# Kernel optimization log

Measured on AMD Instinct MI355X. Metric: run time of the kernel, lower is better.

## Reference

```python
import jax, jax.numpy as jnp
import numpy as np


def setup_inputs() -> dict:
    key = jax.random.key(0)
    ks = jax.random.split(key, 6)
    B, S, H = 1, 512, 2048
    NH, D = 16, 128
    S_CACHE = 8192
    TOPK = 16
    hidden_states = jax.random.normal(ks[0], (B, S, H), dtype=jnp.float32)
    Wqkv = jax.random.normal(ks[1], (3 * H, H), dtype=jnp.float32) * 0.02
    Wout = jax.random.normal(ks[2], (H, H), dtype=jnp.float32) * 0.02
    k_cache = jax.random.normal(ks[3], (B, NH, S_CACHE, D), dtype=jnp.float32)
    v_cache = jax.random.normal(ks[4], (B, NH, S_CACHE, D), dtype=jnp.float32)
    position_bias = jax.random.normal(ks[5], (NH, S, S), dtype=jnp.float32) * 0.1
    # causal mask: True = masked out (matches torch masked_fill semantics)
    attention_mask = ~jnp.tril(jnp.ones((S, S), dtype=bool))
    return {
        "hidden_states": hidden_states,
        "Wqkv": Wqkv,
        "Wout": Wout,
        "k_cache": k_cache,
        "v_cache": v_cache,
        "position_bias": position_bias,
        "attention_mask": attention_mask,
        "topk": TOPK,
    }


SIM_THRESHOLD = 0.25  # config.sim_threshold


def reference(hidden_states, Wqkv, Wout, k_cache, v_cache, position_bias,
              attention_mask, topk):
    B, S, H = hidden_states.shape
    NH, D = k_cache.shape[1], k_cache.shape[3]
    scale = 1.0 / jnp.sqrt(jnp.asarray(D, hidden_states.dtype))

    # QKV projection (Linear, no bias): x @ W^T, then split heads
    qkv = jnp.einsum('bsh,oh->bso', hidden_states, Wqkv)
    q, k, v = jnp.split(qkv, 3, axis=-1)
    def to_heads(x):
        return x.reshape(B, S, NH, D).transpose(0, 2, 1, 3)  # [B,NH,S,D]
    q, k, v = to_heads(q), to_heads(k), to_heads(v)

    # local attention scores + alibi-style bias
    scores_local = jnp.einsum('bhqd,bhkd->bhqk', q, k) * scale
    scores_local = scores_local + position_bias[None]  # [B,NH,S,S]

    # cosine-similarity retrieval over long-range cache
    q_n = q / jnp.linalg.norm(q, axis=-1, keepdims=True)
    k_n = k_cache / jnp.linalg.norm(k_cache, axis=-1, keepdims=True)
    sim = jnp.einsum('bhqd,bhkd->bhqk', q_n, k_n)  # [B,NH,S,S_CACHE]
    val, idx = jax.lax.top_k(sim, topk)            # [B,NH,S,topk]
    reshaped_idx = idx.reshape(B, NH, S * topk)

    # gather retrieved K/V
    sel_k = jnp.take_along_axis(k_cache, reshaped_idx[..., None], axis=2)  # [B,NH,S*topk,D]
    sel_v = jnp.take_along_axis(v_cache, reshaped_idx[..., None], axis=2)

    scores_cache = jnp.einsum('bhqd,bhkd->bhqk', q, sel_k) * scale  # [B,NH,S,S*topk]
    neg = jnp.finfo(scores_cache.dtype).min

    # similarity-threshold mask (mask_by_sim=True)
    sim_mask = ~(val > SIM_THRESHOLD)                       # [B,NH,S,topk]
    sim_mask = sim_mask.reshape(B, NH, 1, S * topk)         # broadcast over queries
    scores_cache = jnp.where(sim_mask, neg, scores_cache)

    # block-diagonal external-memory mask: query i attends only to its own topk slots
    rows = jnp.arange(S)[:, None]
    cols_block = jnp.arange(S * topk)[None, :] // topk
    ext_mask = cols_block != rows                           # [S, S*topk], True = masked

    full_mask = jnp.concatenate([ext_mask, attention_mask], axis=1)  # [S, S*topk+S]
    scores = jnp.concatenate([scores_cache, scores_local], axis=-1)
    scores = jnp.where(full_mask[None, None], neg, scores)

    attn = jax.nn.softmax(scores.astype(jnp.float32), axis=-1).astype(v.dtype)
    values = jnp.concatenate([sel_v, v], axis=2)            # [B,NH,S*topk+S,D]
    ctx = jnp.einsum('bhqk,bhkd->bhqd', attn, values)
    ctx = ctx.transpose(0, 2, 1, 3).reshape(B, S, H)
    attn_output = jnp.einsum('bsh,oh->bso', ctx, Wout)
    return attn_output
```

## Files before the change

### kernel.cpp

```cpp
#include <hip/hip_runtime.h>

typedef _Float16 half8 __attribute__((ext_vector_type(8)));
typedef _Float16 half4 __attribute__((ext_vector_type(4)));
typedef _Float16 half2t __attribute__((ext_vector_type(2)));
typedef float f32x4 __attribute__((ext_vector_type(4)));
typedef float f32x2 __attribute__((ext_vector_type(2)));

#define NHEAD 16
#define SEQ 512
#define DIM 128
#define HID 2048
#define SCACHE 8192
#define CAP 64
#define SCALE 0.08838834764831845f
#define NEG_INF (-__builtin_inff())

__global__ __launch_bounds__(256) void gemm_xwT(const float* __restrict__ A,
                                                const float* __restrict__ B,
                                                float* __restrict__ Cpart,
                                                int K, int gridN, int kslices) {
  __shared__ __align__(16) _Float16 As[128][84];
  __shared__ __align__(16) _Float16 Bs[128][84];
  int b = blockIdx.x;
  int kblk = b % kslices;
  int nm = b / kslices;
  int nblk = nm % gridN, mblk = nm / gridN;
  int N = gridN * 128;
  int kchunk = K / kslices;
  int t = threadIdx.x;
  int lane = t & 63, wid = t >> 6;
  int wm = (wid >> 1) * 64, wn = (wid & 1) * 64;
  f32x4 acc[4][4] = {};
  const float* Ab = A + (size_t)mblk * 128 * K;
  const float* Bb = B + (size_t)nblk * 128 * K;
  int rowS = t >> 4, c4 = (t & 15) * 4;

  for (int k0 = kblk * kchunk; k0 < kblk * kchunk + kchunk; k0 += 64) {
#pragma unroll
    for (int i = 0; i < 8; ++i) {
      int row = rowS + 16 * i;
      float4 av = *(const float4*)(Ab + (size_t)row * K + k0 + c4);
      float4 bv = *(const float4*)(Bb + (size_t)row * K + k0 + c4);
      half4 ah = {(_Float16)av.x, (_Float16)av.y, (_Float16)av.z, (_Float16)av.w};
      half4 bh = {(_Float16)bv.x, (_Float16)bv.y, (_Float16)bv.z, (_Float16)bv.w};
      *(half4*)&As[row][c4] = ah;
      *(half4*)&Bs[row][c4] = bh;
    }
    __syncthreads();
#pragma unroll
    for (int ks = 0; ks < 2; ++ks) {
      int ko = ks * 32 + (lane >> 4) * 8;
      int rr = lane & 15;
      half8 af[4], bf[4];
#pragma unroll
      for (int i = 0; i < 4; ++i) af[i] = *(const half8*)&As[wm + i * 16 + rr][ko];
#pragma unroll
      for (int j = 0; j < 4; ++j) bf[j] = *(const half8*)&Bs[wn + j * 16 + rr][ko];
#pragma unroll
      for (int i = 0; i < 4; ++i)
#pragma unroll
        for (int j = 0; j < 4; ++j)
          acc[i][j] = __builtin_amdgcn_mfma_f32_16x16x32_f16(af[i], bf[j], acc[i][j], 0, 0, 0);
    }
    __syncthreads();
  }
  float* Cp = Cpart + (size_t)kblk * ((size_t)gridN * 128) * 512;
  int cR = (lane >> 4) * 4, cC = lane & 15;
#pragma unroll
  for (int i = 0; i < 4; ++i)
#pragma unroll
    for (int j = 0; j < 4; ++j) {
      int row = mblk * 128 + wm + i * 16 + cR;
      int col = nblk * 128 + wn + j * 16 + cC;
#pragma unroll
      for (int r = 0; r < 4; ++r)
        Cp[(size_t)(row + r) * N + col] = acc[i][j][r];
    }
}

__global__ __launch_bounds__(256) void reduce_k(const float* __restrict__ part,
                                                float* __restrict__ dst,
                                                int kslices, int ncol, int dstride) {
  size_t e = ((size_t)blockIdx.x * 256 + threadIdx.x) * 4;
  size_t slice = (size_t)512 * ncol;
  f32x4 s = *(const f32x4*)(part + e);
  for (int p = 1; p < kslices; ++p)
    s += *(const f32x4*)(part + (size_t)p * slice + e);
  size_t row = e / ncol;
  int col = (int)(e % ncol);
  *(f32x4*)(dst + row * dstride + col) = s;
}

__global__ __launch_bounds__(256) void split_hilo(const float* __restrict__ src,
                                                  _Float16* __restrict__ hi,
                                                  _Float16* __restrict__ lo) {
  size_t e = ((size_t)blockIdx.x * 256 + threadIdx.x) * 4;
  f32x4 v = *(const f32x4*)(src + e);
  half4 h = {(_Float16)v[0], (_Float16)v[1], (_Float16)v[2], (_Float16)v[3]};
  half4 l = {(_Float16)(v[0] - (float)h[0]), (_Float16)(v[1] - (float)h[1]),
             (_Float16)(v[2] - (float)h[2]), (_Float16)(v[3] - (float)h[3])};
  *(half4*)(hi + e) = h;
  *(half4*)(lo + e) = l;
}

__global__ __launch_bounds__(256) void gemm_q_hi(const _Float16* __restrict__ Ahg,
                                                 const _Float16* __restrict__ Alg,
                                                 const _Float16* __restrict__ Bhg,
                                                 const _Float16* __restrict__ Blg,
                                                 float* __restrict__ C) {
  __shared__ __align__(16) _Float16 Ahs[32][72], Als[32][72];
  __shared__ __align__(16) _Float16 Bhs[32][72], Bls[32][72];
  int b = blockIdx.x;
  int nblk = b & 63, mblk = b >> 6;
  int t = threadIdx.x, lane = t & 63, w = t >> 6;
  int wm = (w >> 1) * 16, wn = (w & 1) * 16;
  int quad = lane >> 4, rr = lane & 15;
  f32x4 acc = {};
  const _Float16* Ab0 = Ahg + (size_t)(mblk * 32) * 2048;
  const _Float16* Ab1 = Alg + (size_t)(mblk * 32) * 2048;
  const _Float16* Bb0 = Bhg + (size_t)(nblk * 32) * 2048;
  const _Float16* Bb1 = Blg + (size_t)(nblk * 32) * 2048;
  int srow = t >> 3, sc = (t & 7) * 8;

  for (int k0 = 0; k0 < 2048; k0 += 64) {
    size_t goff = (size_t)srow * 2048 + k0 + sc;
    *(uint4*)&Ahs[srow][sc] = *(const uint4*)(Ab0 + goff);
    *(uint4*)&Als[srow][sc] = *(const uint4*)(Ab1 + goff);
    *(uint4*)&Bhs[srow][sc] = *(const uint4*)(Bb0 + goff);
    *(uint4*)&Bls[srow][sc] = *(const uint4*)(Bb1 + goff);
    __syncthreads();
#pragma unroll
    for (int ks = 0; ks < 2; ++ks) {
      int ko = ks * 32 + quad * 8;
      half8 afh = *(const half8*)&Ahs[wm + rr][ko];
      half8 afl = *(const half8*)&Als[wm + rr][ko];
      half8 bfh = *(const half8*)&Bhs[wn + rr][ko];
      half8 bfl = *(const half8*)&Bls[wn + rr][ko];
      acc = __builtin_amdgcn_mfma_f32_16x16x32_f16(afl, bfh, acc, 0, 0, 0);
      acc = __builtin_amdgcn_mfma_f32_16x16x32_f16(afh, bfl, acc, 0, 0, 0);
      acc = __builtin_amdgcn_mfma_f32_16x16x32_f16(afh, bfh, acc, 0, 0, 0);
    }
    __syncthreads();
  }
  int row = mblk * 32 + wm + quad * 4;
  int col = nblk * 32 + wn + rr;
#pragma unroll
  for (int r = 0; r < 4; ++r)
    C[(size_t)(row + r) * (3 * HID) + col] = acc[r];
}

__global__ __launch_bounds__(256) void cache_norm(const float* __restrict__ kc,
                                                  _Float16* __restrict__ kn16,
                                                  double* __restrict__ kninv) {
  int w = threadIdx.x >> 6, lane = threadIdx.x & 63;
  int row = blockIdx.x * 4 + w;
  f32x2 v = *(const f32x2*)(kc + (size_t)row * DIM + lane * 2);
  double s = (double)v[0] * v[0] + (double)v[1] * v[1];
#pragma unroll
  for (int off = 32; off; off >>= 1) s += __shfl_xor(s, off);
  float inv = rsqrtf((float)s);
  half2t o = {(_Float16)(v[0] * inv), (_Float16)(v[1] * inv)};
  *(half2t*)(kn16 + (size_t)row * DIM + lane * 2) = o;
  if (lane == 0) kninv[row] = 1.0 / sqrt(s);
}

__global__ __launch_bounds__(256) void prep_local(const float* __restrict__ qkv,
                                                  _Float16* __restrict__ q16,
                                                  _Float16* __restrict__ k16,
                                                  _Float16* __restrict__ qn16) {
  int w = threadIdx.x >> 6, lane = threadIdx.x & 63;
  int rid = blockIdx.x * 4 + w;
  int h = rid >> 9, s = rid & 511;
  const float* qp = qkv + (size_t)s * (3 * HID) + h * DIM + lane * 2;
  f32x2 q = *(const f32x2*)qp;
  f32x2 k = *(const f32x2*)(qp + HID);
  float ss = q[0] * q[0] + q[1] * q[1];
#pragma unroll
  for (int off = 32; off; off >>= 1) ss += __shfl_xor(ss, off);
  float inv = rsqrtf(ss);
  half2t qh = {(_Float16)q[0], (_Float16)q[1]};
  half2t kh = {(_Float16)k[0], (_Float16)k[1]};
  half2t qnh = {(_Float16)(q[0] * inv), (_Float16)(q[1] * inv)};
  *(half2t*)(q16 + (size_t)rid * DIM + lane * 2) = qh;
  *(half2t*)(k16 + (size_t)rid * DIM + lane * 2) = kh;
  *(half2t*)(qn16 + (size_t)rid * DIM + lane * 2) = qnh;
}

__global__ __launch_bounds__(256) void sim_cand(const _Float16* __restrict__ qn16,
                                                const _Float16* __restrict__ kn16,
                                                int* __restrict__ cnt,
                                                int* __restrict__ cidx) {
  __shared__ __align__(16) _Float16 Qs[64][132];
  int b = blockIdx.x;
  int h = b & 15, cblk = b >> 4;
  int t = threadIdx.x, lane = t & 63, w = t >> 6;
  int quad = lane >> 4, rr = lane & 15;

  half8 bf[2][4];
  {
    const _Float16* kb = kn16 + ((size_t)(h * SCACHE + cblk * 128 + w * 32)) * DIM;
#pragma unroll
    for (int jn = 0; jn < 2; ++jn)
#pragma unroll
      for (int ks = 0; ks < 4; ++ks)
        bf[jn][ks] = *(const half8*)(kb + (size_t)(jn * 16 + rr) * DIM + ks * 32 + quad * 8);
  }

  for (int qt = 0; qt < 8; ++qt) {
    __syncthreads();
    const _Float16* qb = qn16 + ((size_t)(h * SEQ + qt * 64)) * DIM;
#pragma unroll
    for (int i = 0; i < 4; ++i) {
      int f = t + 256 * i;
      int row = f >> 4, c8 = (f & 15) * 8;
      *(uint4*)&Qs[row][c8] = *(const uint4*)(qb + (size_t)row * DIM + c8);
    }
    __syncthreads();

    f32x4 acc[4][2] = {};
#pragma unroll
    for (int ks = 0; ks < 4; ++ks) {
      int ko = ks * 32 + quad * 8;
      half8 af[4];
#pragma unroll
      for (int i = 0; i < 4; ++i) af[i] = *(const half8*)&Qs[i * 16 + rr][ko];
#pragma unroll
      for (int i = 0; i < 4; ++i)
#pragma unroll
        for (int j = 0; j < 2; ++j)
          acc[i][j] = __builtin_amdgcn_mfma_f32_16x16x32_f16(af[i], bf[j][ks], acc[i][j], 0, 0, 0);
    }
    int qrow_base = qt * 64 + (quad << 2);
    int key_base = cblk * 128 + w * 32 + rr;
#pragma unroll
    for (int i = 0; i < 4; ++i)
#pragma unroll
      for (int j = 0; j < 2; ++j)
#pragma unroll
        for (int r = 0; r < 4; ++r) {
          float v = acc[i][j][r];
          if (v > 0.249f) {
            int q = qrow_base + i * 16 + r;
            int rowid = h * SEQ + q;
            int pos = atomicAdd(&cnt[rowid], 1);
            if (pos < CAP) cidx[rowid * CAP + pos] = key_base + j * 16;
          }
        }
  }
}

__global__ __launch_bounds__(256) void select_topk(const int* __restrict__ cnt,
                                                   const int* __restrict__ cidx,
                                                   const float* __restrict__ qkv,
                                                   const float* __restrict__ kcache,
                                                   const double* __restrict__ kninv,
                                                   int* __restrict__ sel_idx,
                                                   float* __restrict__ sel_score) {
  int w = threadIdx.x >> 6, lane = threadIdx.x & 63;
  int rowid = blockIdx.x * 4 + w;
  int h = rowid >> 9, s = rowid & 511;
  const float* qp = qkv + (size_t)s * (3 * HID) + h * DIM;

  f32x2 qv2 = *(const f32x2*)(qp + lane * 2);
  double qs = (double)qv2[0] * qv2[0] + (double)qv2[1] * qv2[1];
#pragma unroll
  for (int off = 32; off; off >>= 1) qs += __shfl_xor(qs, off);
  double thr = 0.25 * sqrt(qs);

  int n = min(cnt[rowid], CAP);
  int idx = 0x7fffffff;
  double r = -1e300, d = 0.0;
  if (lane < n) {
    idx = cidx[rowid * CAP + lane];
    const float* kp = kcache + ((size_t)(h * SCACHE + idx)) * DIM;
    double d0 = 0.0, d1 = 0.0;
#pragma unroll
    for (int j = 0; j < DIM; j += 8) {
      f32x4 ka = *(const f32x4*)(kp + j);
      f32x4 kb = *(const f32x4*)(kp + j + 4);
      f32x4 qa = *(const f32x4*)(qp + j);
      f32x4 qb = *(const f32x4*)(qp + j + 4);
      d0 = fma((double)qa[0], (double)ka[0], d0);
      d1 = fma((double)qa[1], (double)ka[1], d1);
      d0 = fma((double)qa[2], (double)ka[2], d0);
      d1 = fma((double)qa[3], (double)ka[3], d1);
      d0 = fma((double)qb[0], (double)kb[0], d0);
      d1 = fma((double)qb[1], (double)kb[1], d1);
      d0 = fma((double)qb[2], (double)kb[2], d0);
      d1 = fma((double)qb[3], (double)kb[3], d1);
    }
    d = d0 + d1;
    r = d * kninv[h * SCACHE + idx];
  }

  int rank = 0;
  for (int j = 0; j < n; ++j) {
    double rj = __shfl(r, j);
    int ij = __shfl(idx, j);
    if (rj > r || (rj == r && ij < idx)) ++rank;
  }
  bool sel = (lane < n) && (rank < 16) && (r > thr);
  unsigned long long m = __ballot(sel);
  int nsel = __popcll(m);
  if (sel) {
    int pos = __popcll(m & ((1ull << lane) - 1));
    sel_idx[rowid * 16 + pos] = idx;
    sel_score[rowid * 16 + pos] = (float)(d * (double)SCALE);
  }
  if (lane >= nsel && lane < 16) {
    sel_idx[rowid * 16 + lane] = 0;
    sel_score[rowid * 16 + lane] = NEG_INF;
  }
}

__global__ __launch_bounds__(256) void attn_part(const float* __restrict__ qkv,
                                                 const _Float16* __restrict__ q16,
                                                 const _Float16* __restrict__ k16,
                                                 const float* __restrict__ bias,
                                                 float* __restrict__ part_m,
                                                 float* __restrict__ part_l,
                                                 float* __restrict__ part_o) {
  __shared__ __align__(16) _Float16 Vs[128][136];
  __shared__ __align__(16) _Float16 Ps[16][136];
  __shared__ float mred[16][4], lred[16][4];

  int pb = blockIdx.x;
  int tt = pb % 80, h = pb / 80;
  int qb, cb;
  if (tt < 8)       { qb = tt;                cb = 0; }
  else if (tt < 24) { int u = tt - 8;  qb = 8 + (u >> 1); cb = u & 1; }
  else if (tt < 48) { int u = tt - 24; int q3 = u / 3; qb = 16 + q3; cb = u - q3 * 3; }
  else              { int u = tt - 48; qb = 24 + (u >> 2); cb = u & 3; }
  int q0 = qb * 16, kc0 = cb * 128;

  int t = threadIdx.x, lane = t & 63, w = t >> 6;
  int quad = lane >> 4, col = lane & 15;

  const float* vbase = qkv + 2 * HID + h * DIM;
#pragma unroll
  for (int i = 0; i < 16; ++i) {
    int idx = t + 256 * i;
    int key = idx & 127, dg = idx >> 7;
    f32x4 vv = *(const f32x4*)(vbase + (size_t)(kc0 + key) * (3 * HID) + dg * 4);
#pragma unroll
    for (int e = 0; e < 4; ++e) Vs[dg * 4 + e][key] = (_Float16)vv[e];
  }

  const _Float16* qbp = q16 + ((size_t)(h * SEQ + q0)) * DIM;
  half8 af[4];
#pragma unroll
  for (int ks = 0; ks < 4; ++ks)
    af[ks] = *(const half8*)(qbp + (size_t)col * DIM + ks * 32 + quad * 8);

  f32x4 acc[2] = {};
#pragma unroll
  for (int jn = 0; jn < 2; ++jn) {
    const _Float16* kp = k16 + ((size_t)(h * SEQ + kc0 + w * 32 + jn * 16 + col)) * DIM;
#pragma unroll
    for (int ks = 0; ks < 4; ++ks) {
      half8 bf = *(const half8*)(kp + ks * 32 + quad * 8);
      acc[jn] = __builtin_amdgcn_mfma_f32_16x16x32_f16(af[ks], bf, acc[jn], 0, 0, 0);
    }
  }
  float s[2][4];
#pragma unroll
  for (int jn = 0; jn < 2; ++jn) {
    int keyg = kc0 + w * 32 + jn * 16 + col;
#pragma unroll
    for (int r = 0; r < 4; ++r) {
      int qrow = q0 + quad * 4 + r;
      float sv = NEG_INF;
      if (keyg <= qrow)
        sv = acc[jn][r] * SCALE + bias[((size_t)h * SEQ + qrow) * SEQ + keyg];
      s[jn][r] = sv;
    }
  }

  float mw[4];
#pragma unroll
  for (int r = 0; r < 4; ++r) {
    float m = fmaxf(s[0][r], s[1][r]);
#pragma unroll
    for (int off = 1; off < 16; off <<= 1) m = fmaxf(m, __shfl_xor(m, off));
    mw[r] = m;
  }
  if (col == 0)
#pragma unroll
    for (int r = 0; r < 4; ++r) mred[quad * 4 + r][w] = mw[r];
  __syncthreads();

  float M[4];
#pragma unroll
  for (int r = 0; r < 4; ++r) {
    int row = quad * 4 + r;
    float m = fmaxf(fmaxf(mred[row][0], mred[row][1]),
                    fmaxf(mred[row][2], mred[row][3]));
    M[r] = m;
    float p0 = __expf(s[0][r] - m);
    float p1 = __expf(s[1][r] - m);
    Ps[row][w * 32 + col] = (_Float16)p0;
    Ps[row][w * 32 + 16 + col] = (_Float16)p1;
    float l = p0 + p1;
#pragma unroll
    for (int off = 1; off < 16; off <<= 1) l += __shfl_xor(l, off);
    if (col == 0) lred[row][w] = l;
  }
  if (w == 0 && col == 0)
#pragma unroll
    for (int r = 0; r < 4; ++r) part_m[pb * 16 + quad * 4 + r] = M[r];
  __syncthreads();

  f32x4 o[2] = {};
#pragma unroll
  for (int jn = 0; jn < 2; ++jn) {
#pragma unroll
    for (int ks = 0; ks < 4; ++ks) {
      half8 a = *(const half8*)&Ps[col][ks * 32 + quad * 8];
      half8 bv = *(const half8*)&Vs[w * 32 + jn * 16 + col][ks * 32 + quad * 8];
      o[jn] = __builtin_amdgcn_mfma_f32_16x16x32_f16(a, bv, o[jn], 0, 0, 0);
    }
  }
#pragma unroll
  for (int jn = 0; jn < 2; ++jn)
#pragma unroll
    for (int r = 0; r < 4; ++r)
      part_o[((size_t)pb * 16 + quad * 4 + r) * 128 + w * 32 + jn * 16 + col] = o[jn][r];
  if (t < 16)
    part_l[pb * 16 + t] = lred[t][0] + lred[t][1] + lred[t][2] + lred[t][3];
}

__global__ __launch_bounds__(256) void attn_merge(const float* __restrict__ part_m,
                                                  const float* __restrict__ part_l,
                                                  const float* __restrict__ part_o,
                                                  const int* __restrict__ sel_idx,
                                                  const float* __restrict__ sel_score,
                                                  const float* __restrict__ vcache,
                                                  float* __restrict__ ctx) {
  int w = threadIdx.x >> 6, lane = threadIdx.x & 63;
  int row = blockIdx.x * 4 + w;
  int h = row >> 9, q = row & 511;
  int qb = q >> 4, r = q & 15;
  int base = (qb < 8) ? qb
           : (qb < 16) ? 8 + 2 * (qb - 8)
           : (qb < 24) ? 24 + 3 * (qb - 16)
                       : 48 + 4 * (qb - 24);
  int ncb = (qb >> 3) + 1;
  int pb0 = h * 80 + base;

  float scv[16], mc = NEG_INF;
#pragma unroll
  for (int j = 0; j < 16; ++j) {
    scv[j] = sel_score[row * 16 + j];
    mc = fmaxf(mc, scv[j]);
  }
  float mi[4];
  float M = mc;
  for (int i = 0; i < ncb; ++i) {
    mi[i] = part_m[(pb0 + i) * 16 + r];
    M = fmaxf(M, mi[i]);
  }
  f32x2 O = {0.f, 0.f};
  float L = 0.f;
  for (int i = 0; i < ncb; ++i) {
    float sc = __expf(mi[i] - M);
    f32x2 ov = *(const f32x2*)(part_o + ((size_t)(pb0 + i) * 16 + r) * 128 + lane * 2);
    O += ov * sc;
    L += part_l[(pb0 + i) * 16 + r] * sc;
  }
#pragma unroll
  for (int j = 0; j < 16; ++j) {
    if (scv[j] > NEG_INF) {
      float wv = __expf(scv[j] - M);
      int idx = sel_idx[row * 16 + j];
      f32x2 v = *(const f32x2*)(vcache + ((size_t)(h * SCACHE + idx)) * DIM + lane * 2);
      O += v * wv;
      L += wv;
    }
  }
  f32x2 res = O * (1.f / L);
  *(f32x2*)(ctx + (size_t)q * HID + h * DIM + lane * 2) = res;
}

extern "C" void kernel_launch(void* const* d_in, const int* in_sizes, int n_in,
                              void* d_out, int out_size, void* d_ws, size_t ws_size,
                              hipStream_t stream) {
  const float* hidden = (const float*)d_in[0];
  const float* Wqkv   = (const float*)d_in[1];
  const float* Wout   = (const float*)d_in[2];
  const float* kcache = (const float*)d_in[3];
  const float* vcache = (const float*)d_in[4];
  const float* bias   = (const float*)d_in[5];

  char* ws = (char*)d_ws;
  size_t off = 0;
  float*    qkv   = (float*)(ws + off);    off += (size_t)SEQ * 3 * HID * 4;
  _Float16* q16   = (_Float16*)(ws + off); off += (size_t)NHEAD * SEQ * DIM * 2;
  _Float16* k16   = (_Float16*)(ws + off); off += (size_t)NHEAD * SEQ * DIM * 2;
  _Float16* qn16  = (_Float16*)(ws + off); off += (size_t)NHEAD * SEQ * DIM * 2;
  _Float16* kn16  = (_Float16*)(ws + off); off += (size_t)NHEAD * SCACHE * DIM * 2;
  double*   kninv = (double*)(ws + off);   off += (size_t)NHEAD * SCACHE * 8;
  int*      ccnt  = (int*)(ws + off);      off += (size_t)NHEAD * SEQ * 4;
  int*      cidx  = (int*)(ws + off);      off += (size_t)NHEAD * SEQ * CAP * 4;
  int*      selidx  = (int*)(ws + off);    off += (size_t)NHEAD * SEQ * 16 * 4;
  float*    selsc   = (float*)(ws + off);  off += (size_t)NHEAD * SEQ * 16 * 4;
  float*    ctx   = (float*)(ws + off);    off += (size_t)SEQ * HID * 4;
  float*    pm    = (float*)(ws + off);    off += (size_t)1280 * 16 * 4;
  float*    pl    = (float*)(ws + off);    off += (size_t)1280 * 16 * 4;
  float*    po    = (float*)(ws + off);    off += (size_t)1280 * 16 * 128 * 4;
  float*    gpart = (float*)(ws + off);
  _Float16* Ahg = (_Float16*)gpart;
  _Float16* Alg = Ahg + (size_t)SEQ * HID;
  _Float16* Bhg = Alg + (size_t)SEQ * HID;
  _Float16* Blg = Bhg + (size_t)HID * HID;

  hipMemsetAsync(ccnt, 0, (size_t)NHEAD * SEQ * 4, stream);
  cache_norm<<<dim3(NHEAD * SCACHE / 4), dim3(256), 0, stream>>>(kcache, kn16, kninv);
  gemm_xwT<<<dim3(4 * 32 * 4), dim3(256), 0, stream>>>(hidden, Wqkv + (size_t)2048 * 2048,
                                                       gpart, 2048, 32, 4);
  reduce_k<<<dim3(SEQ * 4096 / 1024), dim3(256), 0, stream>>>(gpart, qkv + 2048, 4, 4096,
                                                              3 * HID);
  split_hilo<<<dim3(SEQ * HID / 1024), dim3(256), 0, stream>>>(hidden, Ahg, Alg);
  split_hilo<<<dim3(HID * HID / 1024), dim3(256), 0, stream>>>(Wqkv, Bhg, Blg);
  gemm_q_hi<<<dim3(1024), dim3(256), 0, stream>>>(Ahg, Alg, Bhg, Blg, qkv);
  prep_local<<<dim3(NHEAD * SEQ / 4), dim3(256), 0, stream>>>(qkv, q16, k16, qn16);
  sim_cand<<<dim3(NHEAD * 64), dim3(256), 0, stream>>>(qn16, kn16, ccnt, cidx);
  select_topk<<<dim3(NHEAD * SEQ / 4), dim3(256), 0, stream>>>(ccnt, cidx, qkv, kcache,
                                                               kninv, selidx, selsc);
  attn_part<<<dim3(16 * 80), dim3(256), 0, stream>>>(qkv, q16, k16, bias, pm, pl, po);
  attn_merge<<<dim3(NHEAD * SEQ / 4), dim3(256), 0, stream>>>(pm, pl, po, selidx, selsc,
                                                              vcache, ctx);
  gemm_xwT<<<dim3(4 * 16 * 8), dim3(256), 0, stream>>>(ctx, Wout, gpart, 2048, 16, 8);
  reduce_k<<<dim3(SEQ * 2048 / 1024), dim3(256), 0, stream>>>(gpart, (float*)d_out, 8, 2048,
                                                              2048);
}
```

Before: 449.7 us.

## Buffer similarity candidates in LDS and merge per head in separate kernel

sim_cand now collects candidate (query, key) pairs into a block-local shared-memory buffer using LDS atomics, instead of doing a global atomicAdd per hit. The buffer is written out per block, and a new cand_merge kernel (one block per head) scatters the records into the per-row candidate lists and writes the counts, so the memset is no longer needed. The Q tile loads are also software-prefetched into registers one iteration ahead. This trades global atomic traffic for an extra launch, a 16-block serial merge pass and an overflow cap of 2048 records per block.

```diff
diff --git a/kernel.cpp b/kernel.cpp
--- a/kernel.cpp
+++ b/kernel.cpp
@@ -14,6 +14,7 @@
 #define CAP 64
 #define SCALE 0.08838834764831845f
 #define NEG_INF (-__builtin_inff())
+#define RECMAX 2048
 
 __global__ __launch_bounds__(256) void gemm_xwT(const float* __restrict__ A,
                                                 const float* __restrict__ B,
@@ -188,13 +189,16 @@
 
 __global__ __launch_bounds__(256) void sim_cand(const _Float16* __restrict__ qn16,
                                                 const _Float16* __restrict__ kn16,
-                                                int* __restrict__ cnt,
-                                                int* __restrict__ cidx) {
+                                                int* __restrict__ rec,
+                                                int* __restrict__ reccnt) {
   __shared__ __align__(16) _Float16 Qs[64][132];
+  __shared__ int ls_buf[RECMAX];
+  __shared__ int ls_cnt;
   int b = blockIdx.x;
   int h = b & 15, cblk = b >> 4;
   int t = threadIdx.x, lane = t & 63, w = t >> 6;
   int quad = lane >> 4, rr = lane & 15;
+  if (t == 0) ls_cnt = 0;
 
   half8 bf[2][4];
   {
@@ -206,14 +210,29 @@
         bf[jn][ks] = *(const half8*)(kb + (size_t)(jn * 16 + rr) * DIM + ks * 32 + quad * 8);
   }
 
+  const _Float16* qbase = qn16 + (size_t)h * SEQ * DIM;
+  int srow = t >> 4, sc8 = (t & 15) * 8;
+  uint4 qreg[4];
+#pragma unroll
+  for (int i = 0; i < 4; ++i) {
+    int f = t + 256 * i;
+    qreg[i] = *(const uint4*)(qbase + (size_t)(f >> 4) * DIM + (f & 15) * 8);
+  }
+
   for (int qt = 0; qt < 8; ++qt) {
     __syncthreads();
-    const _Float16* qb = qn16 + ((size_t)(h * SEQ + qt * 64)) * DIM;
 #pragma unroll
     for (int i = 0; i < 4; ++i) {
       int f = t + 256 * i;
-      int row = f >> 4, c8 = (f & 15) * 8;
-      *(uint4*)&Qs[row][c8] = *(const uint4*)(qb + (size_t)row * DIM + c8);
+      *(uint4*)&Qs[f >> 4][(f & 15) * 8] = qreg[i];
+    }
+    if (qt < 7) {
+      const _Float16* qb = qbase + (size_t)(qt + 1) * 64 * DIM;
+#pragma unroll
+      for (int i = 0; i < 4; ++i) {
+        int f = t + 256 * i;
+        qreg[i] = *(const uint4*)(qb + (size_t)(f >> 4) * DIM + (f & 15) * 8);
+      }
     }
     __syncthreads();
 
@@ -241,12 +260,42 @@
           float v = acc[i][j][r];
           if (v > 0.249f) {
             int q = qrow_base + i * 16 + r;
-            int rowid = h * SEQ + q;
-            int pos = atomicAdd(&cnt[rowid], 1);
-            if (pos < CAP) cidx[rowid * CAP + pos] = key_base + j * 16;
+            int p = atomicAdd(&ls_cnt, 1);
+            if (p < RECMAX) ls_buf[p] = (q << 13) | (key_base + j * 16);
           }
         }
   }
+  __syncthreads();
+  int total = ls_cnt;
+  if (total > RECMAX) total = RECMAX;
+  int* rp = rec + (size_t)b * RECMAX;
+  for (int e = t; e < total; e += 256) rp[e] = ls_buf[e];
+  if (t == 0) reccnt[b] = total;
+}
+
+__global__ __launch_bounds__(256) void cand_merge(const int* __restrict__ rec,
+                                                  const int* __restrict__ reccnt,
+                                                  int* __restrict__ cnt,
+                                                  int* __restrict__ cidx) {
+  __shared__ int lc[512];
+  int h = blockIdx.x;
+  int t = threadIdx.x, w = t >> 6, lane = t & 63;
+  for (int i = t; i < 512; i += 256) lc[i] = 0;
+  __syncthreads();
+  for (int s8 = 0; s8 < 16; ++s8) {
+    int sb = s8 * 4 + w;
+    int bA = sb * 16 + h;
+    int n = reccnt[bA];
+    const int* rp = rec + (size_t)bA * RECMAX;
+    for (int e = lane; e < n; e += 64) {
+      int rv = rp[e];
+      int q = rv >> 13, key = rv & 8191;
+      int pos = atomicAdd(&lc[q], 1);
+      if (pos < CAP) cidx[((size_t)h * 512 + q) * CAP + pos] = key;
+    }
+  }
+  __syncthreads();
+  for (int i = t; i < 512; i += 256) cnt[h * 512 + i] = lc[i];
 }
 
 __global__ __launch_bounds__(256) void select_topk(const int* __restrict__ cnt,
@@ -512,8 +561,9 @@
   _Float16* Alg = Ahg + (size_t)SEQ * HID;
   _Float16* Bhg = Alg + (size_t)SEQ * HID;
   _Float16* Blg = Bhg + (size_t)HID * HID;
-
-  hipMemsetAsync(ccnt, 0, (size_t)NHEAD * SEQ * 4, stream);
+  int*      rec    = (int*)gpart;
+  int*      reccnt = rec + (size_t)1024 * RECMAX;
+
   cache_norm<<<dim3(NHEAD * SCACHE / 4), dim3(256), 0, stream>>>(kcache, kn16, kninv);
   gemm_xwT<<<dim3(4 * 32 * 4), dim3(256), 0, stream>>>(hidden, Wqkv + (size_t)2048 * 2048,
                                                        gpart, 2048, 32, 4);
@@ -523,7 +573,8 @@
   split_hilo<<<dim3(HID * HID / 1024), dim3(256), 0, stream>>>(Wqkv, Bhg, Blg);
   gemm_q_hi<<<dim3(1024), dim3(256), 0, stream>>>(Ahg, Alg, Bhg, Blg, qkv);
   prep_local<<<dim3(NHEAD * SEQ / 4), dim3(256), 0, stream>>>(qkv, q16, k16, qn16);
-  sim_cand<<<dim3(NHEAD * 64), dim3(256), 0, stream>>>(qn16, kn16, ccnt, cidx);
+  sim_cand<<<dim3(NHEAD * 64), dim3(256), 0, stream>>>(qn16, kn16, rec, reccnt);
+  cand_merge<<<dim3(NHEAD), dim3(256), 0, stream>>>(rec, reccnt, ccnt, cidx);
   select_topk<<<dim3(NHEAD * SEQ / 4), dim3(256), 0, stream>>>(ccnt, cidx, qkv, kcache,
                                                                kninv, selidx, selsc);
   attn_part<<<dim3(16 * 80), dim3(256), 0, stream>>>(qkv, q16, k16, bias, pm, pl, po);
```

Result: slower. 460.2 us (+2.3%).
